# Kernel optimization log

Measured on AMD Instinct MI355X. Metric: run time of the kernel, lower is better.

Reference implementation:

```python
import jax, jax.numpy as jnp
import numpy as np
from jax import lax


def setup_inputs() -> dict:
    key = jax.random.key(0)
    k1, k2 = jax.random.split(key)
    B, T, C, U, W = 8, 4096, 512, 512, 2
    inputs = jax.random.normal(k1, (B, T, C), dtype=jnp.float32)
    kernel = jax.random.normal(k2, (W, C, 3 * U), dtype=jnp.float32) * (1.0 / np.sqrt(W * C))
    bias = jnp.zeros((3 * U,), dtype=jnp.float32)
    return {"inputs": inputs, "kernel": kernel, "bias": bias}


def _fo_pool(x, f):
    # x, f: [B, T, U]; c_t = f_t * c_{t-1} + (1 - f_t) * x_t, c_0 = 0
    xT = jnp.swapaxes(x, 0, 1)  # [T, B, U]
    fT = jnp.swapaxes(f, 0, 1)
    c0 = jnp.zeros(x.shape[:1] + x.shape[2:], dtype=x.dtype)  # [B, U]

    def step(c, fx):
        ft, xt = fx
        c = ft * c + (1.0 - ft) * xt
        return c, c

    _, cT = lax.scan(step, c0, (fT, xT))
    return jnp.swapaxes(cT, 0, 1)  # [B, T, U]


def reference(inputs, kernel, bias):
    # Conv1D, padding='same', stride=1, NWC layout
    gates = lax.conv_general_dilated(
        inputs, kernel, window_strides=(1,), padding='SAME',
        dimension_numbers=('NWC', 'WIO', 'NWC')) + bias  # [B, T, 3U]
    x, forget, output = jnp.split(gates, 3, axis=-1)
    x = jnp.tanh(x)
    forget = jax.nn.sigmoid(forget)
    c = _fo_pool(x, forget)
    h = jax.nn.sigmoid(output) * c
    return h
```

## Files before the change

kernel.cpp:

```cpp
#include <hip/hip_runtime.h>

typedef unsigned short u16;
typedef unsigned int u32;
typedef _Float16 f16;
typedef __attribute__((ext_vector_type(8))) _Float16 half8;
typedef __attribute__((ext_vector_type(2))) __fp16 fp16x2;
typedef __attribute__((ext_vector_type(4))) float float4_;
typedef __attribute__((ext_vector_type(4))) unsigned short ushort4_;
typedef __attribute__((ext_vector_type(4))) unsigned int u32x4;

union hu { f16 h; u16 u; };

__device__ __forceinline__ u32 pkrtz(float a, float b) {
    fp16x2 t = __builtin_amdgcn_cvt_pkrtz(a, b);
    union { fp16x2 h; u32 u; } cv; cv.h = t;
    return cv.u;
}

__device__ __forceinline__ void gl16(const u16* g, u16* l) {
    __builtin_amdgcn_global_load_lds(
        (const __attribute__((address_space(1))) void*)g,
        (__attribute__((address_space(3))) void*)l, 16, 0, 0);
}

#define Bsz 8
#define Tsz 4096
#define Csz 512
#define Usz 512
#define NG  1536
#define KK  1024
#define MM  32768
#define NCH 64
#define CHL 64

__global__ void prep_a(const float* __restrict__ in, u16* __restrict__ A16) {
    int gid = blockIdx.x * 256 + threadIdx.x;
    int idx8 = gid * 8;
    int c8 = idx8 & 511;
    int row = idx8 >> 9;
    int b = (u32)row / 4097u;
    int t = row - b * 4097;
    u32x4 w;
    if (t == Tsz) {
        w = (u32x4)0;
    } else {
        const float* p = in + ((size_t)(b * Tsz + t) << 9) + c8;
        float4_ v0 = *(const float4_*)p;
        float4_ v1 = *(const float4_*)(p + 4);
        w.x = pkrtz(v0.x, v0.y); w.y = pkrtz(v0.z, v0.w);
        w.z = pkrtz(v1.x, v1.y); w.w = pkrtz(v1.z, v1.w);
    }
    *(u32x4*)(A16 + idx8) = w;
}

__global__ void prep_k(const float* __restrict__ kern, u16* __restrict__ KT) {
    int n = blockIdx.x * 256 + threadIdx.x;
    int k = blockIdx.y;
    float v = kern[(size_t)k * NG + n];
    hu cv; cv.h = (f16)v;
    KT[(size_t)n * KK + k] = cv.u;
}

__global__ __launch_bounds__(256, 4) void gemm_gates(
    const u16* __restrict__ A16, const u16* __restrict__ KT,
    const float* __restrict__ bias,
    u16* __restrict__ X, u16* __restrict__ F, float* __restrict__ O)
{
    __shared__ u16 lA[8192], lB[8192];

    const int tid  = threadIdx.x;
    const int lane = tid & 63;
    const int wave = tid >> 6;

    const int g   = blockIdx.x;
    const int grp = g / 192;
    const int r   = g - grp * 192;
    const int nb  = r % 12;
    const int mb  = grp * 16 + r / 12;
    const int m0 = mb * 128;
    const int n0 = nb * 128;
    const int b  = m0 >> 12;
    const int t0 = m0 & 4095;
    const int arow0 = b * (Tsz + 1) + t0;

    float4_ acc[4][4];
    #pragma unroll
    for (int i = 0; i < 4; ++i)
        #pragma unroll
        for (int j = 0; j < 4; ++j) acc[i][j] = (float4_)0.0f;

    const int wm = (wave >> 1) * 64;
    const int wn = (wave & 1) * 64;
    const int ar = wm + (lane & 15);
    const int br = wn + (lane & 15);
    const int q  = lane >> 4;
    const int swz = lane & 7;

    for (int kc = 0; kc < KK; kc += 64) {
        __syncthreads();
        const int tap = kc >> 9;
        const int kin = kc & 511;
        const int ab = arow0 + tap;
        #pragma unroll
        for (int it = 0; it < 4; ++it) {
            const int s = it * 256 + tid;
            const int row = s >> 3, p = s & 7;
            const int c = p ^ (row & 7);
            gl16(A16 + (((size_t)(ab + row)) << 9) + kin + c * 8, lA + (s - lane) * 8);
        }
        #pragma unroll
        for (int it = 0; it < 4; ++it) {
            const int s = it * 256 + tid;
            const int row = s >> 3, p = s & 7;
            const int c = p ^ (row & 7);
            gl16(KT + (((size_t)(n0 + row)) << 10) + kc + c * 8, lB + (s - lane) * 8);
        }
        __syncthreads();

        #pragma unroll
        for (int s2 = 0; s2 < 2; ++s2) {
            half8 fa[4], fb[4];
            const int cc = (s2 * 4 + q) ^ swz;
            #pragma unroll
            for (int i = 0; i < 4; ++i) {
                fa[i] = *(const half8*)(lA + (ar + i * 16) * 64 + cc * 8);
                fb[i] = *(const half8*)(lB + (br + i * 16) * 64 + cc * 8);
            }
            #pragma unroll
            for (int mi = 0; mi < 4; ++mi)
                #pragma unroll
                for (int ni = 0; ni < 4; ++ni)
                    acc[mi][ni] = __builtin_amdgcn_mfma_f32_16x16x32_f16(fa[mi], fb[ni], acc[mi][ni], 0, 0, 0);
        }
    }

    const int plane = nb >> 2;
    const int rq = q * 4;
    const int cl = lane & 15;
    #pragma unroll
    for (int mi = 0; mi < 4; ++mi)
        #pragma unroll
        for (int ni = 0; ni < 4; ++ni) {
            const int gm = m0 + wm + mi * 16 + rq;
            const int gn = n0 + wn + ni * 16 + cl;
            const float bv = bias[gn];
            const int cp = gn & 511;
            #pragma unroll
            for (int r2 = 0; r2 < 4; ++r2) {
                float v = acc[mi][ni][r2] + bv;
                if (plane == 0) {
                    float res = 1.0f - 2.0f / (__expf(2.0f * v) + 1.0f);
                    hu cv; cv.h = (f16)res;
                    X[(size_t)(gm + r2) * Usz + cp] = cv.u;
                } else if (plane == 1) {
                    float res = 1.0f / (1.0f + __expf(-v));
                    hu cv; cv.h = (f16)res;
                    F[(size_t)(gm + r2) * Usz + cp] = cv.u;
                } else {
                    float res = 1.0f / (1.0f + __expf(-v));
                    O[(size_t)(gm + r2) * Usz + cp] = res;
                }
            }
        }
}

__device__ __forceinline__ float4_ x4(const u16* p) {
    ushort4_ xr = *(const ushort4_*)p;
    float4_ xv;
    #pragma unroll
    for (int j = 0; j < 4; ++j) { hu cv; cv.u = xr[j]; xv[j] = (float)cv.h; }
    return xv;
}

__global__ void scan_chunk(const u16* __restrict__ F, const u16* __restrict__ X,
                           float* __restrict__ CA, float* __restrict__ CB) {
    int g = blockIdx.x * 256 + threadIdx.x;
    int u4 = (g & 127) * 4;
    int bc = g >> 7;
    size_t base = (size_t)bc * CHL * Usz + u4;
    float4_ c = (float4_)0.0f, A = (float4_)1.0f;
    for (int i = 0; i < CHL; ++i) {
        float4_ fv = x4(F + base + (size_t)i * Usz);
        float4_ xv = x4(X + base + (size_t)i * Usz);
        c = fv * c + (1.0f - fv) * xv;
        A = A * fv;
    }
    *(float4_*)(CA + (size_t)bc * Usz + u4) = A;
    *(float4_*)(CB + (size_t)bc * Usz + u4) = c;
}

__global__ void scan_prefix(const float* __restrict__ CA, const float* __restrict__ CB,
                            float* __restrict__ CS) {
    int g = blockIdx.x * 256 + threadIdx.x;
    int u = g & 511;
    int b = g >> 9;
    float c = 0.0f;
    #pragma unroll 16
    for (int ch = 0; ch < NCH; ++ch) {
        int idx = (b * NCH + ch) * Usz + u;
        CS[idx] = c;
        c = CA[idx] * c + CB[idx];
    }
}

__global__ void scan_final(const u16* __restrict__ F, const u16* __restrict__ X,
                           const float* __restrict__ CS, float* __restrict__ out) {
    int g = blockIdx.x * 256 + threadIdx.x;
    int u4 = (g & 127) * 4;
    int bc = g >> 7;
    size_t base = (size_t)bc * CHL * Usz + u4;
    float4_ c = *(const float4_*)(CS + (size_t)bc * Usz + u4);
    for (int i = 0; i < CHL; ++i) {
        float4_ fv = x4(F + base + (size_t)i * Usz);
        float4_ xv = x4(X + base + (size_t)i * Usz);
        c = fv * c + (1.0f - fv) * xv;
        float4_ ov = *(const float4_*)(out + base + (size_t)i * Usz);
        *(float4_*)(out + base + (size_t)i * Usz) = ov * c;
    }
}

extern "C" void kernel_launch(void* const* d_in, const int* in_sizes, int n_in,
                              void* d_out, int out_size, void* d_ws, size_t ws_size,
                              hipStream_t stream) {
    const float* in   = (const float*)d_in[0];
    const float* kern = (const float*)d_in[1];
    const float* bias = (const float*)d_in[2];
    float* out = (float*)d_out;
    char* ws = (char*)d_ws;

    const size_t A16_B  = (size_t)Bsz * (Tsz + 1) * Csz * 2;
    const size_t OFF_KT = A16_B;
    const size_t OFF_F  = OFF_KT + (size_t)NG * KK * 2;
    const size_t OFF_X  = OFF_F + (size_t)MM * Usz * 2;
    const size_t OFF_CA = OFF_X + (size_t)MM * Usz * 2;
    const size_t CH_B   = (size_t)Bsz * NCH * Usz * 4;
    const size_t NEED   = OFF_CA + 3 * CH_B;

    if (ws_size < NEED) return;

    u16*   A16 = (u16*)ws;
    u16*   KT  = (u16*)(ws + OFF_KT);
    u16*   Fh  = (u16*)(ws + OFF_F);
    u16*   Xb  = (u16*)(ws + OFF_X);
    float* CA  = (float*)(ws + OFF_CA);
    float* CB  = CA + CH_B / 4;
    float* CS  = CB + CH_B / 4;

    prep_a<<<(int)(A16_B / 16 / 256), 256, 0, stream>>>(in, A16);
    prep_k<<<dim3(NG / 256, KK), 256, 0, stream>>>(kern, KT);
    gemm_gates<<<(MM / 128) * (NG / 128), 256, 0, stream>>>(A16, KT, bias, Xb, Fh, out);
    scan_chunk<<<Bsz * NCH * Usz / 4 / 256, 256, 0, stream>>>(Fh, Xb, CA, CB);
    scan_prefix<<<Bsz * Usz / 256, 256, 0, stream>>>(CA, CB, CS);
    scan_final<<<Bsz * NCH * Usz / 4 / 256, 256, 0, stream>>>(Fh, Xb, CS, out);
}
```

Measured before the change: 307.5 us.

## Pipeline GEMM with triple-buffered LDS, 128x256 tiles, tiled weight transpose, finer scan chunks

The gates GEMM now uses 512-thread blocks computing 128x256 tiles, with triple-buffered LDS, global-to-LDS prefetch two k-steps ahead, split MFMA phases using setprio, and an XCD-aware block remap. The weight transpose kernel now goes through shared memory for coalesced reads and writes. The scan uses 128 chunks of 32 steps, and the chunk buffers reuse the A16 workspace region because A16 is no longer needed after the GEMM. These changes target GEMM memory latency and the poor access pattern of the transpose, but they use much more LDS per block and add manual waitcnt logic that could be fragile.

New measurement: 317.0 us. +3.1%, slower.

```diff
diff --git a/kernel.cpp b/kernel.cpp
--- a/kernel.cpp
+++ b/kernel.cpp
@@ -30,8 +30,8 @@
 #define NG  1536
 #define KK  1024
 #define MM  32768
-#define NCH 64
-#define CHL 64
+#define NCH 128
+#define CHL 32
 
 __global__ void prep_a(const float* __restrict__ in, u16* __restrict__ A16) {
     int gid = blockIdx.x * 256 + threadIdx.x;
@@ -54,31 +54,71 @@
 }
 
 __global__ void prep_k(const float* __restrict__ kern, u16* __restrict__ KT) {
-    int n = blockIdx.x * 256 + threadIdx.x;
-    int k = blockIdx.y;
-    float v = kern[(size_t)k * NG + n];
-    hu cv; cv.h = (f16)v;
-    KT[(size_t)n * KK + k] = cv.u;
-}
-
-__global__ __launch_bounds__(256, 4) void gemm_gates(
+    __shared__ u16 t[64][70];
+    const int k0 = blockIdx.x * 64;
+    const int n0 = blockIdx.y * 64;
+    const int tid = threadIdx.x;
+    #pragma unroll
+    for (int it = 0; it < 16; ++it) {
+        int s = it * 256 + tid;
+        int r = s >> 6;
+        int c = s & 63;
+        float v = kern[(size_t)(k0 + r) * NG + n0 + c];
+        hu cv; cv.h = (f16)v;
+        t[c][r] = cv.u;
+    }
+    __syncthreads();
+    #pragma unroll
+    for (int it = 0; it < 4; ++it) {
+        int s = it * 256 + tid;
+        int n = s >> 4;
+        int kq = (s & 15) * 4;
+        ushort4_ w;
+        w.x = t[n][kq]; w.y = t[n][kq + 1]; w.z = t[n][kq + 2]; w.w = t[n][kq + 3];
+        *(ushort4_*)(KT + (size_t)(n0 + n) * KK + k0 + kq) = w;
+    }
+}
+
+#define LDS_A 8192
+#define LDS_B 16384
+
+__device__ __forceinline__ void stage_A(const u16* __restrict__ A16, u16* dst,
+                                        int arow_base, int kin, int tid, int lane) {
+    #pragma unroll
+    for (int it = 0; it < 2; ++it) {
+        int s = it * 512 + tid;
+        int row = s >> 3, p = s & 7;
+        int c = p ^ (row & 7);
+        gl16(A16 + (((size_t)(arow_base + row)) << 9) + kin + c * 8, dst + (s - lane) * 8);
+    }
+}
+
+__device__ __forceinline__ void stage_B_it(const u16* __restrict__ KT, u16* dst,
+                                           int n0, int kc, int it, int tid, int lane) {
+    int s = it * 512 + tid;
+    int row = s >> 3, p = s & 7;
+    int c = p ^ (row & 7);
+    gl16(KT + (((size_t)(n0 + row)) << 10) + kc + c * 8, dst + (s - lane) * 8);
+}
+
+__global__ __launch_bounds__(512, 2) void gemm_gates(
     const u16* __restrict__ A16, const u16* __restrict__ KT,
     const float* __restrict__ bias,
     u16* __restrict__ X, u16* __restrict__ F, float* __restrict__ O)
 {
-    __shared__ u16 lA[8192], lB[8192];
+    __shared__ u16 lA[3 * LDS_A];
+    __shared__ u16 lB[3 * LDS_B];
 
     const int tid  = threadIdx.x;
     const int lane = tid & 63;
     const int wave = tid >> 6;
 
-    const int g   = blockIdx.x;
-    const int grp = g / 192;
-    const int r   = g - grp * 192;
-    const int nb  = r % 12;
-    const int mb  = grp * 16 + r / 12;
+    const int orig = blockIdx.x;
+    const int wg = (orig & 7) * 192 + (orig >> 3);
+    const int nb = wg % 6;
+    const int mb = wg / 6;
     const int m0 = mb * 128;
-    const int n0 = nb * 128;
+    const int n0 = nb * 256;
     const int b  = m0 >> 12;
     const int t0 = m0 & 4095;
     const int arow0 = b * (Tsz + 1) + t0;
@@ -89,52 +129,89 @@
         #pragma unroll
         for (int j = 0; j < 4; ++j) acc[i][j] = (float4_)0.0f;
 
-    const int wm = (wave >> 1) * 64;
-    const int wn = (wave & 1) * 64;
-    const int ar = wm + (lane & 15);
-    const int br = wn + (lane & 15);
-    const int q  = lane >> 4;
+    const int wm = (wave >> 2) * 64;
+    const int wn = (wave & 3) * 64;
+    const int arow = wm + (lane & 15);
+    const int brow = wn + (lane & 15);
+    const int q   = lane >> 4;
     const int swz = lane & 7;
 
-    for (int kc = 0; kc < KK; kc += 64) {
-        __syncthreads();
-        const int tap = kc >> 9;
-        const int kin = kc & 511;
-        const int ab = arow0 + tap;
-        #pragma unroll
-        for (int it = 0; it < 4; ++it) {
-            const int s = it * 256 + tid;
-            const int row = s >> 3, p = s & 7;
-            const int c = p ^ (row & 7);
-            gl16(A16 + (((size_t)(ab + row)) << 9) + kin + c * 8, lA + (s - lane) * 8);
+    stage_A(A16, lA, arow0, 0, tid, lane);
+    #pragma unroll
+    for (int it = 0; it < 4; ++it) stage_B_it(KT, lB, n0, 0, it, tid, lane);
+    stage_A(A16, lA + LDS_A, arow0, 64, tid, lane);
+    #pragma unroll
+    for (int it = 0; it < 4; ++it) stage_B_it(KT, lB + LDS_B, n0, 64, it, tid, lane);
+
+    int buf = 0;
+    #pragma unroll 1
+    for (int kt = 0; kt < 16; ++kt) {
+        if (kt < 15) asm volatile("s_waitcnt vmcnt(6)" ::: "memory");
+        else         asm volatile("s_waitcnt vmcnt(0)" ::: "memory");
+        __builtin_amdgcn_s_barrier();
+
+        const u16* a  = lA + buf * LDS_A;
+        const u16* bs = lB + buf * LDS_B;
+        const int nbuf = (buf >= 1) ? buf - 1 : 2;
+        const int kt2 = kt + 2;
+        const bool st = kt2 < 16;
+        const int kc2 = kt2 * 64;
+
+        half8 fa[4][2], fb01[2][2];
+        #pragma unroll
+        for (int mi = 0; mi < 4; ++mi)
+            #pragma unroll
+            for (int s2 = 0; s2 < 2; ++s2)
+                fa[mi][s2] = *(const half8*)(a + (arow + mi * 16) * 64 + (((s2 * 4 + q) ^ swz) * 8));
+        #pragma unroll
+        for (int ni = 0; ni < 2; ++ni)
+            #pragma unroll
+            for (int s2 = 0; s2 < 2; ++s2)
+                fb01[ni][s2] = *(const half8*)(bs + (brow + ni * 16) * 64 + (((s2 * 4 + q) ^ swz) * 8));
+        if (st) {
+            stage_A(A16, lA + nbuf * LDS_A, arow0 + (kt2 >> 3), (kt2 & 7) * 64, tid, lane);
+            stage_B_it(KT, lB + nbuf * LDS_B, n0, kc2, 0, tid, lane);
         }
-        #pragma unroll
-        for (int it = 0; it < 4; ++it) {
-            const int s = it * 256 + tid;
-            const int row = s >> 3, p = s & 7;
-            const int c = p ^ (row & 7);
-            gl16(KT + (((size_t)(n0 + row)) << 10) + kc + c * 8, lB + (s - lane) * 8);
-        }
-        __syncthreads();
-
-        #pragma unroll
-        for (int s2 = 0; s2 < 2; ++s2) {
-            half8 fa[4], fb[4];
-            const int cc = (s2 * 4 + q) ^ swz;
-            #pragma unroll
-            for (int i = 0; i < 4; ++i) {
-                fa[i] = *(const half8*)(lA + (ar + i * 16) * 64 + cc * 8);
-                fb[i] = *(const half8*)(lB + (br + i * 16) * 64 + cc * 8);
-            }
+        __builtin_amdgcn_s_barrier();
+        asm volatile("s_waitcnt lgkmcnt(0)" ::: "memory");
+        __builtin_amdgcn_s_setprio(1);
+        #pragma unroll
+        for (int s2 = 0; s2 < 2; ++s2)
             #pragma unroll
             for (int mi = 0; mi < 4; ++mi)
                 #pragma unroll
-                for (int ni = 0; ni < 4; ++ni)
-                    acc[mi][ni] = __builtin_amdgcn_mfma_f32_16x16x32_f16(fa[mi], fb[ni], acc[mi][ni], 0, 0, 0);
+                for (int ni = 0; ni < 2; ++ni)
+                    acc[mi][ni] = __builtin_amdgcn_mfma_f32_16x16x32_f16(fa[mi][s2], fb01[ni][s2], acc[mi][ni], 0, 0, 0);
+        __builtin_amdgcn_s_setprio(0);
+        __builtin_amdgcn_s_barrier();
+
+        half8 fb23[2][2];
+        #pragma unroll
+        for (int ni = 0; ni < 2; ++ni)
+            #pragma unroll
+            for (int s2 = 0; s2 < 2; ++s2)
+                fb23[ni][s2] = *(const half8*)(bs + (brow + 32 + ni * 16) * 64 + (((s2 * 4 + q) ^ swz) * 8));
+        if (st) {
+            stage_B_it(KT, lB + nbuf * LDS_B, n0, kc2, 1, tid, lane);
+            stage_B_it(KT, lB + nbuf * LDS_B, n0, kc2, 2, tid, lane);
+            stage_B_it(KT, lB + nbuf * LDS_B, n0, kc2, 3, tid, lane);
         }
-    }
-
-    const int plane = nb >> 2;
+        __builtin_amdgcn_s_barrier();
+        asm volatile("s_waitcnt lgkmcnt(0)" ::: "memory");
+        __builtin_amdgcn_s_setprio(1);
+        #pragma unroll
+        for (int s2 = 0; s2 < 2; ++s2)
+            #pragma unroll
+            for (int mi = 0; mi < 4; ++mi)
+                #pragma unroll
+                for (int ni = 0; ni < 2; ++ni)
+                    acc[mi][ni + 2] = __builtin_amdgcn_mfma_f32_16x16x32_f16(fa[mi][s2], fb23[ni][s2], acc[mi][ni + 2], 0, 0, 0);
+        __builtin_amdgcn_s_setprio(0);
+
+        buf = (buf == 2) ? 0 : buf + 1;
+    }
+
+    const int plane = nb >> 1;
     const int rq = q * 4;
     const int cl = lane & 15;
     #pragma unroll
@@ -232,9 +309,7 @@
     const size_t OFF_KT = A16_B;
     const size_t OFF_F  = OFF_KT + (size_t)NG * KK * 2;
     const size_t OFF_X  = OFF_F + (size_t)MM * Usz * 2;
-    const size_t OFF_CA = OFF_X + (size_t)MM * Usz * 2;
-    const size_t CH_B   = (size_t)Bsz * NCH * Usz * 4;
-    const size_t NEED   = OFF_CA + 3 * CH_B;
+    const size_t NEED   = OFF_X + (size_t)MM * Usz * 2;
 
     if (ws_size < NEED) return;
 
@@ -242,13 +317,14 @@
     u16*   KT  = (u16*)(ws + OFF_KT);
     u16*   Fh  = (u16*)(ws + OFF_F);
     u16*   Xb  = (u16*)(ws + OFF_X);
-    float* CA  = (float*)(ws + OFF_CA);
-    float* CB  = CA + CH_B / 4;
-    float* CS  = CB + CH_B / 4;
+    const size_t CH = (size_t)Bsz * NCH * Usz;
+    float* CA = (float*)ws;
+    float* CB = CA + CH;
+    float* CS = CB + CH;
 
     prep_a<<<(int)(A16_B / 16 / 256), 256, 0, stream>>>(in, A16);
-    prep_k<<<dim3(NG / 256, KK), 256, 0, stream>>>(kern, KT);
-    gemm_gates<<<(MM / 128) * (NG / 128), 256, 0, stream>>>(A16, KT, bias, Xb, Fh, out);
+    prep_k<<<dim3(KK / 64, NG / 64), 256, 0, stream>>>(kern, KT);
+    gemm_gates<<<(MM / 128) * (NG / 256), 512, 0, stream>>>(A16, KT, bias, Xb, Fh, out);
     scan_chunk<<<Bsz * NCH * Usz / 4 / 256, 256, 0, stream>>>(Fh, Xb, CA, CB);
     scan_prefix<<<Bsz * Usz / 256, 256, 0, stream>>>(CA, CB, CS);
     scan_final<<<Bsz * NCH * Usz / 4 / 256, 256, 0, stream>>>(Fh, Xb, CS, out);
```

## Tile kernel transpose via LDS, remap GEMM blocks per XCD, halve scan chunks

Applied to the files above, without the earlier changes.

The kernel-weight transpose now goes through a 64x64 LDS tile, so reads from global memory and writes to KT are both coalesced, replacing a scattered per-element write. GEMM workgroup IDs are remapped so consecutive blocks on each of 8 XCDs cover contiguous M-tiles, which should improve L2 reuse of A and KT. Scan chunk length drops from 64 to 32, doubling the parallelism of the chunk and final passes at the cost of a longer serial prefix. Scan scratch buffers now reuse the A16 region, which is dead after the GEMM, shrinking the workspace requirement.

Measured after the change: 292.6 us. -4.9%, faster.

```diff
diff --git a/kernel.cpp b/kernel.cpp
--- a/kernel.cpp
+++ b/kernel.cpp
@@ -30,8 +30,8 @@
 #define NG  1536
 #define KK  1024
 #define MM  32768
-#define NCH 64
-#define CHL 64
+#define NCH 128
+#define CHL 32
 
 __global__ void prep_a(const float* __restrict__ in, u16* __restrict__ A16) {
     int gid = blockIdx.x * 256 + threadIdx.x;
@@ -54,11 +54,29 @@
 }
 
 __global__ void prep_k(const float* __restrict__ kern, u16* __restrict__ KT) {
-    int n = blockIdx.x * 256 + threadIdx.x;
-    int k = blockIdx.y;
-    float v = kern[(size_t)k * NG + n];
-    hu cv; cv.h = (f16)v;
-    KT[(size_t)n * KK + k] = cv.u;
+    __shared__ u16 t[64][70];
+    const int k0 = blockIdx.x * 64;
+    const int n0 = blockIdx.y * 64;
+    const int tid = threadIdx.x;
+    #pragma unroll
+    for (int it = 0; it < 16; ++it) {
+        int s = it * 256 + tid;
+        int r = s >> 6;
+        int c = s & 63;
+        float v = kern[(size_t)(k0 + r) * NG + n0 + c];
+        hu cv; cv.h = (f16)v;
+        t[c][r] = cv.u;
+    }
+    __syncthreads();
+    #pragma unroll
+    for (int it = 0; it < 4; ++it) {
+        int s = it * 256 + tid;
+        int n = s >> 4;
+        int kq = (s & 15) * 4;
+        ushort4_ w;
+        w.x = t[n][kq]; w.y = t[n][kq + 1]; w.z = t[n][kq + 2]; w.w = t[n][kq + 3];
+        *(ushort4_*)(KT + (size_t)(n0 + n) * KK + k0 + kq) = w;
+    }
 }
 
 __global__ __launch_bounds__(256, 4) void gemm_gates(
@@ -72,11 +90,10 @@
     const int lane = tid & 63;
     const int wave = tid >> 6;
 
-    const int g   = blockIdx.x;
-    const int grp = g / 192;
-    const int r   = g - grp * 192;
-    const int nb  = r % 12;
-    const int mb  = grp * 16 + r / 12;
+    const int orig = blockIdx.x;
+    const int wg = (orig & 7) * 384 + (orig >> 3);
+    const int nb = wg % 12;
+    const int mb = wg / 12;
     const int m0 = mb * 128;
     const int n0 = nb * 128;
     const int b  = m0 >> 12;
@@ -232,9 +249,7 @@
     const size_t OFF_KT = A16_B;
     const size_t OFF_F  = OFF_KT + (size_t)NG * KK * 2;
     const size_t OFF_X  = OFF_F + (size_t)MM * Usz * 2;
-    const size_t OFF_CA = OFF_X + (size_t)MM * Usz * 2;
-    const size_t CH_B   = (size_t)Bsz * NCH * Usz * 4;
-    const size_t NEED   = OFF_CA + 3 * CH_B;
+    const size_t NEED   = OFF_X + (size_t)MM * Usz * 2;
 
     if (ws_size < NEED) return;
 
@@ -242,12 +257,13 @@
     u16*   KT  = (u16*)(ws + OFF_KT);
     u16*   Fh  = (u16*)(ws + OFF_F);
     u16*   Xb  = (u16*)(ws + OFF_X);
-    float* CA  = (float*)(ws + OFF_CA);
-    float* CB  = CA + CH_B / 4;
-    float* CS  = CB + CH_B / 4;
+    const size_t CH = (size_t)Bsz * NCH * Usz;
+    float* CA = (float*)ws;
+    float* CB = CA + CH;
+    float* CS = CB + CH;
 
     prep_a<<<(int)(A16_B / 16 / 256), 256, 0, stream>>>(in, A16);
-    prep_k<<<dim3(NG / 256, KK), 256, 0, stream>>>(kern, KT);
+    prep_k<<<dim3(KK / 64, NG / 64), 256, 0, stream>>>(kern, KT);
     gemm_gates<<<(MM / 128) * (NG / 128), 256, 0, stream>>>(A16, KT, bias, Xb, Fh, out);
     scan_chunk<<<Bsz * NCH * Usz / 4 / 256, 256, 0, stream>>>(Fh, Xb, CA, CB);
     scan_prefix<<<Bsz * Usz / 256, 256, 0, stream>>>(CA, CB, CS);
```
